# Performance work log

Hardware: AMD Instinct MI355X
Metric: run time of the kernel (lower is better)

## Reference

```python
import jax, jax.numpy as jnp
import numpy as np

B, T, C = 2, 2048, 2048
H, Hk, D = 32, 4, 64
N_REP = H // Hk
THETA = 10000.0


def _rope_tables():
    inv_freq = 1.0 / (THETA ** (np.arange(0, D, 2, dtype=np.float64) / D))  # [D/2]
    t = np.arange(T, dtype=np.float64)
    freqs = np.outer(t, inv_freq)                # [T, D/2]
    emb = np.repeat(freqs, 2, axis=-1)           # interleaved [T, D]
    return jnp.asarray(np.cos(emb), jnp.float32), jnp.asarray(np.sin(emb), jnp.float32)


def setup_inputs() -> dict:
    key = jax.random.key(0)
    kx, kq, kk, kv, ko = jax.random.split(key, 5)
    scale = 0.02
    x = jax.random.normal(kx, (B, T, C), jnp.float32)
    wq = jax.random.normal(kq, (H * D, C), jnp.float32) * scale
    wk = jax.random.normal(kk, (Hk * D, C), jnp.float32) * scale
    wv = jax.random.normal(kv, (Hk * D, C), jnp.float32) * scale
    wo = jax.random.normal(ko, (C, H * D), jnp.float32) * scale
    cos, sin = _rope_tables()
    return {"x": x, "cos": cos, "sin": sin, "wq": wq, "wk": wk, "wv": wv, "wo": wo}


def _apply_rope(x, cos, sin):
    # x: [B, h, T, D]; cos/sin: [T, D] interleaved
    x1 = x[..., 0::2]
    x2 = x[..., 1::2]
    rot = jnp.stack([-x2, x1], axis=-1).reshape(x.shape)
    return x * cos[None, None] + rot * sin[None, None]


def reference(x, cos, sin, wq, wk, wv, wo):
    q = (x @ wq.T).reshape(B, T, H, D).transpose(0, 2, 1, 3)    # [B,H,T,D]
    k = (x @ wk.T).reshape(B, T, Hk, D).transpose(0, 2, 1, 3)   # [B,Hk,T,D]
    v = (x @ wv.T).reshape(B, T, Hk, D).transpose(0, 2, 1, 3)   # [B,Hk,T,D]
    q = _apply_rope(q, cos, sin)
    k = _apply_rope(k, cos, sin)
    # new_cache = (k, v) pre-repeat
    kr = jnp.repeat(k, N_REP, axis=1)                            # [B,H,T,D]
    vr = jnp.repeat(v, N_REP, axis=1)
    scores = jnp.einsum('bhtd,bhsd->bhts', q, kr) / jnp.sqrt(jnp.float32(D))
    mask = jnp.tril(jnp.ones((T, T), dtype=bool))                # causal (kv_cache is None)
    scores = jnp.where(mask, scores, jnp.finfo(scores.dtype).min)
    attn = jax.nn.softmax(scores, axis=-1)
    o = jnp.einsum('bhts,bhsd->bhtd', attn, vr)
    o = o.transpose(0, 2, 1, 3).reshape(B, T, H * D)
    return (o @ wo.T, k, v)
```

## Files before the change

kernel.cpp:

```cpp
#include <hip/hip_runtime.h>
#include <hip/hip_bf16.h>

#define B_ 2
#define T_ 2048
#define C_ 2048
#define H_ 32
#define HK_ 4
#define D_ 64

typedef __attribute__((ext_vector_type(4)))  float f32x4;
typedef __attribute__((ext_vector_type(2)))  float f32x2;
typedef __attribute__((ext_vector_type(16))) float f32x16;
typedef __attribute__((ext_vector_type(8)))  short bf16x8;

static __device__ __forceinline__ unsigned short f2bf(float f) {
  union { __hip_bfloat16 h; unsigned short s; } u;
  u.h = __float2bfloat16(f);
  return u.s;
}
static __device__ __forceinline__ float bf2f(unsigned short s) {
  union { unsigned int u; float f; } u; u.u = ((unsigned int)s) << 16; return u.f;
}
static __device__ __forceinline__ unsigned int cvtpk(float lo, float hi) {
  unsigned int r;
  asm("v_cvt_pk_bf16_f32 %0, %1, %2" : "=v"(r) : "v"(lo), "v"(hi));
  return r;
}

#define GLD16(gp, lp) __builtin_amdgcn_global_load_lds( \
    (const __attribute__((address_space(1))) unsigned int*)(gp), \
    (__attribute__((address_space(3))) unsigned int*)(unsigned int)(uintptr_t)(lp), 16, 0, 0)

__global__ void f32_to_bf16(const float* __restrict__ src, unsigned short* __restrict__ dst, int n4) {
  const int i = blockIdx.x * blockDim.x + threadIdx.x;
  if (i >= n4) return;
  f32x4 v = *(const f32x4*)(src + 4 * (size_t)i);
  ushort4 o;
  o.x = f2bf(v[0]); o.y = f2bf(v[1]); o.z = f2bf(v[2]); o.w = f2bf(v[3]);
  *(ushort4*)(dst + 4 * (size_t)i) = o;
}

template<bool BF16OUT>
__global__ __launch_bounds__(512, 2)
void gemm256(const unsigned short* __restrict__ A, const unsigned short* __restrict__ W,
             void* __restrict__ Cout, int M, int N, int K) {
  __shared__ unsigned short As[2][128 * 64];
  __shared__ unsigned short Bs[2][256 * 64];

  const int tid  = threadIdx.x;
  const int lane = tid & 63;
  const int w    = tid >> 6;
  const int wm   = w >> 2;
  const int wn   = w & 3;
  const int g    = lane >> 4;
  const int lr   = lane & 15;

  const int bm = blockIdx.y * 128;
  const int bn = blockIdx.x * 256;

  const int sr8 = lane >> 3;
  const int sch = (lane & 7) ^ sr8;
  const unsigned short* Ag = A + (size_t)(bm + w * 8 + sr8) * K + sch * 8;
  const unsigned short* Wg = W + (size_t)(bn + w * 8 + sr8) * K + sch * 8;

#define STG(buf, k0) do { \
    GLD16(Ag + (k0),                   &As[buf][(      w * 8) * 64]); \
    GLD16(Ag + (size_t)64  * K + (k0), &As[buf][(64  + w * 8) * 64]); \
    GLD16(Wg + (k0),                   &Bs[buf][(      w * 8) * 64]); \
    GLD16(Wg + (size_t)64  * K + (k0), &Bs[buf][(64  + w * 8) * 64]); \
    GLD16(Wg + (size_t)128 * K + (k0), &Bs[buf][(128 + w * 8) * 64]); \
    GLD16(Wg + (size_t)192 * K + (k0), &Bs[buf][(192 + w * 8) * 64]); \
  } while (0)

  f32x4 acc[4][4] = {};
  const int nt = K >> 6;
  STG(0, 0);

  for (int t = 0; t < nt; ++t) {
    const int p = t & 1;
    asm volatile("s_waitcnt vmcnt(0)" ::: "memory");
    __builtin_amdgcn_s_barrier();
    if (t + 1 < nt) STG(p ^ 1, (t + 1) << 6);

    const unsigned short* At = &As[p][0];
    const unsigned short* Bt = &Bs[p][0];
#pragma unroll
    for (int kh = 0; kh < 2; ++kh) {
      bf16x8 af[4], wf[4];
#pragma unroll
      for (int m = 0; m < 4; m++) {
        const int row = wm * 64 + m * 16 + lr;
        af[m] = *(const bf16x8*)&At[row * 64 + (((g + 4 * kh) ^ (row & 7)) << 3)];
      }
#pragma unroll
      for (int n = 0; n < 4; n++) {
        const int row = wn * 64 + n * 16 + lr;
        wf[n] = *(const bf16x8*)&Bt[row * 64 + (((g + 4 * kh) ^ (row & 7)) << 3)];
      }
      __builtin_amdgcn_s_setprio(1);
#pragma unroll
      for (int m = 0; m < 4; m++)
#pragma unroll
        for (int n = 0; n < 4; n++)
          acc[m][n] = __builtin_amdgcn_mfma_f32_16x16x32_bf16(af[m], wf[n], acc[m][n], 0, 0, 0);
      __builtin_amdgcn_s_setprio(0);
    }
  }
#undef STG

#pragma unroll
  for (int m = 0; m < 4; m++) {
    const int row = bm + wm * 64 + m * 16 + g * 4;
#pragma unroll
    for (int n = 0; n < 4; n++) {
      const int col = bn + wn * 64 + n * 16 + lr;
#pragma unroll
      for (int r = 0; r < 4; r++) {
        if (BF16OUT)
          ((unsigned short*)Cout)[(size_t)(row + r) * N + col] = f2bf(acc[m][n][r]);
        else
          ((float*)Cout)[(size_t)(row + r) * N + col] = acc[m][n][r];
      }
    }
  }
}

__global__ void gqa_rope_q(const unsigned short* __restrict__ qkv,
                           const float* __restrict__ cosT,
                           const float* __restrict__ sinT,
                           unsigned short* __restrict__ qb) {
  const int idx = blockIdx.x * blockDim.x + threadIdx.x;
  const int i  = idx & 31;
  const int h  = (idx >> 5) & 31;
  const int bt = idx >> 10;
  const int t  = bt & (T_ - 1);
  const int b  = bt >> 11;

  const unsigned int qv = *(const unsigned int*)(qkv + (size_t)bt * 2560 + h * D_ + 2 * i);
  const float x1 = bf2f((unsigned short)(qv & 0xffff));
  const float x2 = bf2f((unsigned short)(qv >> 16));
  const float c = cosT[t * D_ + 2 * i];
  const float s = sinT[t * D_ + 2 * i];
  const float o0 = x1 * c - x2 * s;
  const float o1 = x2 * c + x1 * s;
  const size_t o = ((size_t)(b * H_ + h) * T_ + t) * D_ + 2 * i;
  *(unsigned int*)(qb + o) = (unsigned int)f2bf(o0) | ((unsigned int)f2bf(o1) << 16);
}

__global__ void gqa_rope_k(const unsigned short* __restrict__ qkv,
                           const float* __restrict__ cosT,
                           const float* __restrict__ sinT,
                           float* __restrict__ kout,
                           unsigned short* __restrict__ kb) {
  const int idx = blockIdx.x * blockDim.x + threadIdx.x;
  const int i  = idx & 31;
  const int hk = (idx >> 5) & 3;
  const int bt = idx >> 7;
  const int t  = bt & (T_ - 1);
  const int b  = bt >> 11;

  const unsigned int kv = *(const unsigned int*)(qkv + (size_t)bt * 2560 + 2048 + hk * D_ + 2 * i);
  const float x1 = bf2f((unsigned short)(kv & 0xffff));
  const float x2 = bf2f((unsigned short)(kv >> 16));
  const float c = cosT[t * D_ + 2 * i];
  const float s = sinT[t * D_ + 2 * i];
  const float o0 = x1 * c - x2 * s;
  const float o1 = x2 * c + x1 * s;
  const size_t o = ((size_t)(b * HK_ + hk) * T_ + t) * D_ + 2 * i;
  f32x2 ov; ov[0] = o0; ov[1] = o1;
  *(f32x2*)(kout + o) = ov;
  *(unsigned int*)(kb + o) = (unsigned int)f2bf(o0) | ((unsigned int)f2bf(o1) << 16);
}

__global__ void gqa_v_reorder(const unsigned short* __restrict__ qkv,
                              float* __restrict__ vout,
                              unsigned short* __restrict__ vt) {
  const int idx = blockIdx.x * blockDim.x + threadIdx.x;
  const int d  = idx & 63;
  const int hk = (idx >> 6) & 3;
  const int bt = idx >> 8;
  const int t  = bt & (T_ - 1);
  const int b  = bt >> 11;

  const unsigned short v = qkv[(size_t)bt * 2560 + 2304 + hk * D_ + d];
  vout[((size_t)(b * HK_ + hk) * T_ + t) * D_ + d] = bf2f(v);

  const int tm   = t & 15;
  const int tpos = (t & ~15) | ((tm & 3) + ((tm >> 3) << 2) + ((tm & 4) << 1));
  vt[((size_t)(b * HK_ + hk) * D_ + d) * T_ + tpos] = v;
}

__global__ __launch_bounds__(512, 4)
void gqa_attn4(const unsigned short* __restrict__ qb,
               const unsigned short* __restrict__ kb,
               const unsigned short* __restrict__ vt,
               unsigned short* __restrict__ ob) {
  __shared__ unsigned short Ks[3][4096];
  __shared__ unsigned short Vs[3][4096];

  const int tid  = threadIdx.x;
  const int lane = tid & 63;
  const int w    = tid >> 6;
  const int qi   = lane & 31;
  const int hi   = lane >> 5;

  const int qt = 63 - (int)(blockIdx.x >> 3);
  const int go = blockIdx.x & 7;
  const int b  = go >> 2;
  const int hk = go & 3;
  const int h  = hk * 8 + w;
  const int bh = b * H_ + h;

  const int qbase = qt * 32;
  const int qrow  = qbase + qi;

  const unsigned short* qptr = qb + ((size_t)bh * T_ + qrow) * D_ + 8 * hi;
  bf16x8 qf[4];
#pragma unroll
  for (int c = 0; c < 4; c++) qf[c] = *(const bf16x8*)(qptr + 16 * c);

  const int srow   = lane >> 3;
  const int schunk = (lane & 7) ^ srow;
  const int krow   = 8 * w + srow;
  const unsigned short* gK = kb + (size_t)(b * HK_ + hk) * T_ * D_ + (size_t)krow * D_ + schunk * 8;
  const unsigned short* gV = vt + (size_t)(b * HK_ + hk) * D_ * T_ + (size_t)krow * T_ + schunk * 8;
  unsigned short* ldsK = &Ks[0][w * 512];
  unsigned short* ldsV = &Vs[0][w * 512];

#define STAGE_KV(pp, kk0) do { \
    GLD16(gK + (size_t)(kk0) * D_, ldsK + (pp) * 4096); \
    GLD16(gV + (kk0),              ldsV + (pp) * 4096); \
  } while (0)

  f32x16 o0 = {}, o1 = {};
  float m = -1e30f, l = 0.f;
  float c1 = 0.f;
  const float SC   = 0.125f * 1.44269504089f;
  const float THRR = 44.3614195f;
  const int   swz  = qi & 7;

  const int nt = ((qbase + 31) >> 6) + 1;
  STAGE_KV(0, 0);
  if (nt > 1) STAGE_KV(1, 64);

  int p = 0;
  for (int it = 0; it < nt; ++it) {
    const int kb0 = it * 64;
    const bool last = (it == nt - 1);
    const bool has1 = (kb0 + 32 <= qbase + 31);

    asm volatile("s_waitcnt lgkmcnt(0)" ::: "memory");
    if (it + 1 < nt) asm volatile("s_waitcnt vmcnt(2)" ::: "memory");
    else             asm volatile("s_waitcnt vmcnt(0)" ::: "memory");
    asm volatile("s_barrier" ::: "memory");
    if (it + 2 < nt) STAGE_KV((p + 2 > 2) ? p - 1 : p + 2, kb0 + 128);

    const unsigned short* Kt = &Ks[0][0] + p * 4096;
    const unsigned short* Vt = &Vs[0][0] + p * 4096;

    f32x16 st0 = {}, st1 = {};
    __builtin_amdgcn_s_setprio(1);
#pragma unroll
    for (int c = 0; c < 4; c++) {
      bf16x8 kf = *(const bf16x8*)&Kt[qi * 64 + (((hi + 2 * c) ^ swz) << 3)];
      st0 = __builtin_amdgcn_mfma_f32_32x32x16_bf16(kf, qf[c], st0, 0, 0, 0);
    }
    if (!last || has1) {
#pragma unroll
      for (int c = 0; c < 4; c++) {
        bf16x8 kf = *(const bf16x8*)&Kt[(32 + qi) * 64 + (((hi + 2 * c) ^ swz) << 3)];
        st1 = __builtin_amdgcn_mfma_f32_32x32x16_bf16(kf, qf[c], st1, 0, 0, 0);
      }
    }
    __builtin_amdgcn_s_setprio(0);

    if (last) {
#pragma unroll
      for (int r = 0; r < 16; ++r) {
        const int key = kb0 + (r & 3) + 8 * (r >> 2) + 4 * hi;
        st0[r] = (key      <= qrow) ? st0[r] : -1e30f;
        st1[r] = (key + 32 <= qrow) ? st1[r] : -1e30f;
      }
    }

    float tmax = fmaxf(st0[0], st0[1]);
#pragma unroll
    for (int r = 2; r < 16; ++r) tmax = fmaxf(tmax, st0[r]);
#pragma unroll
    for (int r = 0; r < 16; ++r) tmax = fmaxf(tmax, st1[r]);
    tmax = fmaxf(tmax, __shfl_xor(tmax, 32));

    if (!__all(tmax <= m + THRR)) {
      const float mnew  = fmaxf(m, tmax);
      const float al    = __builtin_amdgcn_exp2f((m - mnew) * SC);
#pragma unroll
      for (int r = 0; r < 16; ++r) { o0[r] *= al; o1[r] *= al; }
      l *= al;
      m  = mnew;
      c1 = -m * SC;
    }

    float sum = 0.f;
#pragma unroll
    for (int r = 0; r < 16; ++r) { float pv = __builtin_amdgcn_exp2f(__builtin_fmaf(st0[r], SC, c1)); st0[r] = pv; sum += pv; }
#pragma unroll
    for (int r = 0; r < 16; ++r) { float pv = __builtin_amdgcn_exp2f(__builtin_fmaf(st1[r], SC, c1)); st1[r] = pv; sum += pv; }
    sum += __shfl_xor(sum, 32);
    l += sum;

    union U8 { bf16x8 v; unsigned int u[4]; };
    U8 pf[4];
#pragma unroll
    for (int j = 0; j < 4; ++j) {
      pf[0].u[j] = cvtpk(st0[2 * j],     st0[2 * j + 1]);
      pf[1].u[j] = cvtpk(st0[8 + 2 * j], st0[8 + 2 * j + 1]);
      pf[2].u[j] = cvtpk(st1[2 * j],     st1[2 * j + 1]);
      pf[3].u[j] = cvtpk(st1[8 + 2 * j], st1[8 + 2 * j + 1]);
    }

    const int ncf = (!last || has1) ? 4 : 2;
    __builtin_amdgcn_s_setprio(1);
#pragma unroll
    for (int dh = 0; dh < 2; ++dh) {
      const unsigned short* Vrow = &Vt[(dh * 32 + qi) * 64];
      f32x16 oc = dh ? o1 : o0;
#pragma unroll
      for (int c = 0; c < 4; ++c) {
        if (c >= ncf) break;
        bf16x8 vf = *(const bf16x8*)&Vrow[(((2 * c + hi) ^ swz) << 3)];
        oc = __builtin_amdgcn_mfma_f32_32x32x16_bf16(vf, pf[c].v, oc, 0, 0, 0);
      }
      if (dh) o1 = oc; else o0 = oc;
    }
    __builtin_amdgcn_s_setprio(0);

    p = (p > 1) ? 0 : p + 1;
  }

  const float inv = 1.0f / l;
  unsigned short* orow = ob + (size_t)(b * T_ + qrow) * (H_ * D_) + h * D_;
#pragma unroll
  for (int dh = 0; dh < 2; ++dh) {
    const f32x16 ov = dh ? o1 : o0;
#pragma unroll
    for (int rg = 0; rg < 4; ++rg) {
      const int d0 = 32 * dh + 8 * rg + 4 * hi;
      ushort4 pk;
      pk.x = f2bf(ov[4 * rg + 0] * inv);
      pk.y = f2bf(ov[4 * rg + 1] * inv);
      pk.z = f2bf(ov[4 * rg + 2] * inv);
      pk.w = f2bf(ov[4 * rg + 3] * inv);
      *(ushort4*)(orow + d0) = pk;
    }
  }
#undef STAGE_KV
}

extern "C" void kernel_launch(void* const* d_in, const int* in_sizes, int n_in,
                              void* d_out, int out_size, void* d_ws, size_t ws_size,
                              hipStream_t stream) {
  const float* x    = (const float*)d_in[0];
  const float* cosT = (const float*)d_in[1];
  const float* sinT = (const float*)d_in[2];
  const float* wq   = (const float*)d_in[3];
  const float* wk   = (const float*)d_in[4];
  const float* wv   = (const float*)d_in[5];
  const float* wo   = (const float*)d_in[6];

  float* y    = (float*)d_out;
  float* kout = (float*)d_out + (size_t)B_ * T_ * C_;
  float* vout = kout + (size_t)B_ * HK_ * T_ * D_;

  char* ws = (char*)d_ws;
  unsigned short* x_bf   = (unsigned short*)(ws);
  unsigned short* q_bf   = x_bf;
  unsigned short* wqkv   = (unsigned short*)(ws + 16777216);
  unsigned short* k_bf   = wqkv;
  unsigned short* v_t    = (unsigned short*)(ws + 18874368);
  unsigned short* qkv_bf = (unsigned short*)(ws + 27262976);
  unsigned short* o_bf   = qkv_bf;
  unsigned short* wo_bf  = (unsigned short*)(ws + 48234496);

  const int M = B_ * T_;

  f32_to_bf16<<<8192, 256, 0, stream>>>(x,  x_bf, 2097152);
  f32_to_bf16<<<4096, 256, 0, stream>>>(wq, wqkv,                 1048576);
  f32_to_bf16<<<512,  256, 0, stream>>>(wk, wqkv + 2048 * 2048,   131072);
  f32_to_bf16<<<512,  256, 0, stream>>>(wv, wqkv + 2304 * 2048,   131072);

  gemm256<true><<<dim3(2560 / 256, M / 128), 512, 0, stream>>>(x_bf, wqkv, qkv_bf, M, 2560, C_);

  gqa_rope_q<<<16384, 256, 0, stream>>>(qkv_bf, cosT, sinT, q_bf);
  gqa_rope_k<<<2048,  256, 0, stream>>>(qkv_bf, cosT, sinT, kout, k_bf);
  gqa_v_reorder<<<4096, 256, 0, stream>>>(qkv_bf, vout, v_t);

  f32_to_bf16<<<4096, 256, 0, stream>>>(wo, wo_bf, 1048576);

  gqa_attn4<<<512, 512, 0, stream>>>(q_bf, k_bf, v_t, o_bf);

  gemm256<false><<<dim3(C_ / 256, M / 128), 512, 0, stream>>>(o_bf, wo_bf, y, M, C_, H_ * D_);
}
```

Before: 206.8 us.

## Fuse RoPE and K/V reordering into QKV GEMM epilogue with 128x128 tiles

The QKV projection GEMM now applies RoPE to Q and K in its epilogue. It uses a lane shuffle to fetch the paired element, then writes q/k/v directly in the head-major and transposed layouts that attention expects. This removes three elementwise kernels and the round trip through an intermediate qkv buffer. Both GEMMs also move from 128x256 tiles with 512 threads to 128x128 tiles with 256 threads, which doubles the block count. The cost is scattered, poorly coalesced epilogue stores and fp32 cos/sin loads per element inside the GEMM.

After: 198.7 us. -3.9%, faster.

```diff
diff --git a/kernel.cpp b/kernel.cpp
--- a/kernel.cpp
+++ b/kernel.cpp
@@ -40,23 +40,27 @@
   *(ushort4*)(dst + 4 * (size_t)i) = o;
 }
 
-template<bool BF16OUT>
-__global__ __launch_bounds__(512, 2)
-void gemm256(const unsigned short* __restrict__ A, const unsigned short* __restrict__ W,
-             void* __restrict__ Cout, int M, int N, int K) {
+template<int EPI>
+__global__ __launch_bounds__(256, 2)
+void gemm128(const unsigned short* __restrict__ A, const unsigned short* __restrict__ W,
+             int M, int N, int K,
+             float* __restrict__ Cf,
+             const float* __restrict__ cosT, const float* __restrict__ sinT,
+             unsigned short* __restrict__ qb, unsigned short* __restrict__ kbf,
+             unsigned short* __restrict__ vtb, float* __restrict__ koutf,
+             float* __restrict__ voutf) {
   __shared__ unsigned short As[2][128 * 64];
-  __shared__ unsigned short Bs[2][256 * 64];
+  __shared__ unsigned short Bs[2][128 * 64];
 
   const int tid  = threadIdx.x;
   const int lane = tid & 63;
   const int w    = tid >> 6;
-  const int wm   = w >> 2;
-  const int wn   = w & 3;
+  const int wm   = w >> 1, wn = w & 1;
   const int g    = lane >> 4;
   const int lr   = lane & 15;
 
   const int bm = blockIdx.y * 128;
-  const int bn = blockIdx.x * 256;
+  const int bn = blockIdx.x * 128;
 
   const int sr8 = lane >> 3;
   const int sch = (lane & 7) ^ sr8;
@@ -64,12 +68,14 @@
   const unsigned short* Wg = W + (size_t)(bn + w * 8 + sr8) * K + sch * 8;
 
 #define STG(buf, k0) do { \
-    GLD16(Ag + (k0),                   &As[buf][(      w * 8) * 64]); \
-    GLD16(Ag + (size_t)64  * K + (k0), &As[buf][(64  + w * 8) * 64]); \
-    GLD16(Wg + (k0),                   &Bs[buf][(      w * 8) * 64]); \
-    GLD16(Wg + (size_t)64  * K + (k0), &Bs[buf][(64  + w * 8) * 64]); \
-    GLD16(Wg + (size_t)128 * K + (k0), &Bs[buf][(128 + w * 8) * 64]); \
-    GLD16(Wg + (size_t)192 * K + (k0), &Bs[buf][(192 + w * 8) * 64]); \
+    GLD16(Ag + (k0),                   &As[buf][(     w * 8) * 64]); \
+    GLD16(Ag + (size_t)32  * K + (k0), &As[buf][(32 + w * 8) * 64]); \
+    GLD16(Ag + (size_t)64  * K + (k0), &As[buf][(64 + w * 8) * 64]); \
+    GLD16(Ag + (size_t)96  * K + (k0), &As[buf][(96 + w * 8) * 64]); \
+    GLD16(Wg + (k0),                   &Bs[buf][(     w * 8) * 64]); \
+    GLD16(Wg + (size_t)32  * K + (k0), &Bs[buf][(32 + w * 8) * 64]); \
+    GLD16(Wg + (size_t)64  * K + (k0), &Bs[buf][(64 + w * 8) * 64]); \
+    GLD16(Wg + (size_t)96  * K + (k0), &Bs[buf][(96 + w * 8) * 64]); \
   } while (0)
 
   f32x4 acc[4][4] = {};
@@ -108,86 +114,58 @@
   }
 #undef STG
 
-#pragma unroll
-  for (int m = 0; m < 4; m++) {
-    const int row = bm + wm * 64 + m * 16 + g * 4;
-#pragma unroll
-    for (int n = 0; n < 4; n++) {
-      const int col = bn + wn * 64 + n * 16 + lr;
-#pragma unroll
-      for (int r = 0; r < 4; r++) {
-        if (BF16OUT)
-          ((unsigned short*)Cout)[(size_t)(row + r) * N + col] = f2bf(acc[m][n][r]);
-        else
-          ((float*)Cout)[(size_t)(row + r) * N + col] = acc[m][n][r];
+  if (EPI == 0) {
+#pragma unroll
+    for (int m = 0; m < 4; m++) {
+      const int row = bm + wm * 64 + m * 16 + g * 4;
+#pragma unroll
+      for (int n = 0; n < 4; n++) {
+        const int col = bn + wn * 64 + n * 16 + lr;
+#pragma unroll
+        for (int r = 0; r < 4; r++)
+          Cf[(size_t)(row + r) * N + col] = acc[m][n][r];
+      }
+    }
+  } else {
+    const int seg = (bn < 2048) ? 0 : (bn < 2304 ? 1 : 2);
+#pragma unroll
+    for (int m = 0; m < 4; m++) {
+#pragma unroll
+      for (int n = 0; n < 4; n++) {
+        const int col = bn + wn * 64 + n * 16 + lr;
+        const int d   = col & 63;
+#pragma unroll
+        for (int r = 0; r < 4; r++) {
+          const int row = bm + wm * 64 + m * 16 + g * 4 + r;
+          const int tt  = row & (T_ - 1);
+          const int bb  = row >> 11;
+          const float val = acc[m][n][r];
+          if (seg == 2) {
+            const int hk = (col >> 6) - 36;
+            const size_t idx = ((size_t)(bb * HK_ + hk) * T_ + tt) * D_ + d;
+            voutf[idx] = val;
+            const int tm   = tt & 15;
+            const int tpos = (tt & ~15) | ((tm & 3) + ((tm >> 3) << 2) + ((tm & 4) << 1));
+            vtb[((size_t)(bb * HK_ + hk) * D_ + d) * T_ + tpos] = f2bf(val);
+          } else {
+            const float cs = cosT[tt * D_ + d];
+            const float sn = sinT[tt * D_ + d];
+            const float other = __shfl_xor(val, 1);
+            const float o = val * cs + ((lr & 1) ? other : -other) * sn;
+            if (seg == 0) {
+              const int h = col >> 6;
+              qb[((size_t)(bb * H_ + h) * T_ + tt) * D_ + d] = f2bf(o);
+            } else {
+              const int hk = (col >> 6) - 32;
+              const size_t idx = ((size_t)(bb * HK_ + hk) * T_ + tt) * D_ + d;
+              koutf[idx] = o;
+              kbf[idx]   = f2bf(o);
+            }
+          }
+        }
       }
     }
   }
-}
-
-__global__ void gqa_rope_q(const unsigned short* __restrict__ qkv,
-                           const float* __restrict__ cosT,
-                           const float* __restrict__ sinT,
-                           unsigned short* __restrict__ qb) {
-  const int idx = blockIdx.x * blockDim.x + threadIdx.x;
-  const int i  = idx & 31;
-  const int h  = (idx >> 5) & 31;
-  const int bt = idx >> 10;
-  const int t  = bt & (T_ - 1);
-  const int b  = bt >> 11;
-
-  const unsigned int qv = *(const unsigned int*)(qkv + (size_t)bt * 2560 + h * D_ + 2 * i);
-  const float x1 = bf2f((unsigned short)(qv & 0xffff));
-  const float x2 = bf2f((unsigned short)(qv >> 16));
-  const float c = cosT[t * D_ + 2 * i];
-  const float s = sinT[t * D_ + 2 * i];
-  const float o0 = x1 * c - x2 * s;
-  const float o1 = x2 * c + x1 * s;
-  const size_t o = ((size_t)(b * H_ + h) * T_ + t) * D_ + 2 * i;
-  *(unsigned int*)(qb + o) = (unsigned int)f2bf(o0) | ((unsigned int)f2bf(o1) << 16);
-}
-
-__global__ void gqa_rope_k(const unsigned short* __restrict__ qkv,
-                           const float* __restrict__ cosT,
-                           const float* __restrict__ sinT,
-                           float* __restrict__ kout,
-                           unsigned short* __restrict__ kb) {
-  const int idx = blockIdx.x * blockDim.x + threadIdx.x;
-  const int i  = idx & 31;
-  const int hk = (idx >> 5) & 3;
-  const int bt = idx >> 7;
-  const int t  = bt & (T_ - 1);
-  const int b  = bt >> 11;
-
-  const unsigned int kv = *(const unsigned int*)(qkv + (size_t)bt * 2560 + 2048 + hk * D_ + 2 * i);
-  const float x1 = bf2f((unsigned short)(kv & 0xffff));
-  const float x2 = bf2f((unsigned short)(kv >> 16));
-  const float c = cosT[t * D_ + 2 * i];
-  const float s = sinT[t * D_ + 2 * i];
-  const float o0 = x1 * c - x2 * s;
-  const float o1 = x2 * c + x1 * s;
-  const size_t o = ((size_t)(b * HK_ + hk) * T_ + t) * D_ + 2 * i;
-  f32x2 ov; ov[0] = o0; ov[1] = o1;
-  *(f32x2*)(kout + o) = ov;
-  *(unsigned int*)(kb + o) = (unsigned int)f2bf(o0) | ((unsigned int)f2bf(o1) << 16);
-}
-
-__global__ void gqa_v_reorder(const unsigned short* __restrict__ qkv,
-                              float* __restrict__ vout,
-                              unsigned short* __restrict__ vt) {
-  const int idx = blockIdx.x * blockDim.x + threadIdx.x;
-  const int d  = idx & 63;
-  const int hk = (idx >> 6) & 3;
-  const int bt = idx >> 8;
-  const int t  = bt & (T_ - 1);
-  const int b  = bt >> 11;
-
-  const unsigned short v = qkv[(size_t)bt * 2560 + 2304 + hk * D_ + d];
-  vout[((size_t)(b * HK_ + hk) * T_ + t) * D_ + d] = bf2f(v);
-
-  const int tm   = t & 15;
-  const int tpos = (t & ~15) | ((tm & 3) + ((tm >> 3) << 2) + ((tm & 4) << 1));
-  vt[((size_t)(b * HK_ + hk) * D_ + d) * T_ + tpos] = v;
 }
 
 __global__ __launch_bounds__(512, 4)
@@ -372,31 +350,27 @@
   float* vout = kout + (size_t)B_ * HK_ * T_ * D_;
 
   char* ws = (char*)d_ws;
-  unsigned short* x_bf   = (unsigned short*)(ws);
-  unsigned short* q_bf   = x_bf;
-  unsigned short* wqkv   = (unsigned short*)(ws + 16777216);
-  unsigned short* k_bf   = wqkv;
-  unsigned short* v_t    = (unsigned short*)(ws + 18874368);
-  unsigned short* qkv_bf = (unsigned short*)(ws + 27262976);
-  unsigned short* o_bf   = qkv_bf;
-  unsigned short* wo_bf  = (unsigned short*)(ws + 48234496);
+  unsigned short* x_bf = (unsigned short*)(ws);
+  unsigned short* o_bf = x_bf;
+  unsigned short* wqkv = (unsigned short*)(ws + 16777216);
+  unsigned short* q_bf = (unsigned short*)(ws + 27262976);
+  unsigned short* k_bf = (unsigned short*)(ws + 44040192);
+  unsigned short* v_t  = (unsigned short*)(ws + 46137344);
+  unsigned short* wo_bf= (unsigned short*)(ws + 48234496);
 
   const int M = B_ * T_;
 
   f32_to_bf16<<<8192, 256, 0, stream>>>(x,  x_bf, 2097152);
-  f32_to_bf16<<<4096, 256, 0, stream>>>(wq, wqkv,                 1048576);
-  f32_to_bf16<<<512,  256, 0, stream>>>(wk, wqkv + 2048 * 2048,   131072);
-  f32_to_bf16<<<512,  256, 0, stream>>>(wv, wqkv + 2304 * 2048,   131072);
-
-  gemm256<true><<<dim3(2560 / 256, M / 128), 512, 0, stream>>>(x_bf, wqkv, qkv_bf, M, 2560, C_);
-
-  gqa_rope_q<<<16384, 256, 0, stream>>>(qkv_bf, cosT, sinT, q_bf);
-  gqa_rope_k<<<2048,  256, 0, stream>>>(qkv_bf, cosT, sinT, kout, k_bf);
-  gqa_v_reorder<<<4096, 256, 0, stream>>>(qkv_bf, vout, v_t);
-
-  f32_to_bf16<<<4096, 256, 0, stream>>>(wo, wo_bf, 1048576);
+  f32_to_bf16<<<4096, 256, 0, stream>>>(wq, wqkv,               1048576);
+  f32_to_bf16<<<512,  256, 0, stream>>>(wk, wqkv + 2048 * 2048, 131072);
+  f32_to_bf16<<<512,  256, 0, stream>>>(wv, wqkv + 2304 * 2048, 131072);
+  f32_to_bf16<<<4096, 256, 0, stream>>>(wo, wo_bf,              1048576);
+
+  gemm128<1><<<dim3(2560 / 128, M / 128), 256, 0, stream>>>(
+      x_bf, wqkv, M, 2560, C_, nullptr, cosT, sinT, q_bf, k_bf, v_t, kout, vout);
 
   gqa_attn4<<<512, 512, 0, stream>>>(q_bf, k_bf, v_t, o_bf);
 
-  gemm256<false><<<dim3(C_ / 256, M / 128), 512, 0, stream>>>(o_bf, wo_bf, y, M, C_, H_ * D_);
-}
+  gemm128<0><<<dim3(C_ / 128, M / 128), 256, 0, stream>>>(
+      o_bf, wo_bf, M, C_, H_ * D_, y, nullptr, nullptr, nullptr, nullptr, nullptr, nullptr, nullptr);
+}
```
